# Performance work log

Measured on AMD Instinct MI355X. Metric: run time of the kernel, lower is better.

Reference implementation:

```python
import jax, jax.numpy as jnp
import numpy as np

T_SEG = 8      # n_segment
KSZ = 3        # LAM temporal kernel size
PAD = 1        # LAM temporal padding
BN_EPS = 1e-5


def setup_inputs() -> dict:
    key = jax.random.key(0)
    ks = jax.random.split(key, 12)
    n, t, c, h, w = 8, T_SEG, 256, 56, 56
    return {
        "x": jax.random.normal(ks[0], (n * t, c, h, w), jnp.float32),
        "net_w": jax.random.normal(ks[1], (c, c, 3, 3), jnp.float32) * 0.02,
        "net_b": jax.random.normal(ks[2], (c,), jnp.float32) * 0.02,
        "lam_w": jax.random.normal(ks[3], (c, c), jnp.float32) * 0.02,
        "lam_b": jax.random.normal(ks[4], (c,), jnp.float32) * 0.02,
        "mlp_w1": jax.random.normal(ks[5], (2 * t, t), jnp.float32) * 0.3,
        "bn_gamma": jax.random.uniform(ks[6], (2 * t,), jnp.float32, 0.5, 1.5),
        "bn_beta": jax.random.normal(ks[7], (2 * t,), jnp.float32) * 0.1,
        "bn_mean": jax.random.normal(ks[8], (2 * t,), jnp.float32) * 0.1,
        "bn_var": jax.random.uniform(ks[9], (2 * t,), jnp.float32, 0.5, 1.5),
        "mlp_w2": jax.random.normal(ks[10], (KSZ, 2 * t), jnp.float32) * 0.3,
        "me_w": jax.random.normal(ks[11], (3,), jnp.float32) * 0.3,
    }


def reference(x, net_w, net_b, lam_w, lam_b, mlp_w1, bn_gamma, bn_beta,
              bn_mean, bn_var, mlp_w2, me_w):
    t = T_SEG
    nt, c, h, w = x.shape
    n = nt // t

    # --- wrapped net: Conv2d 3x3, pad 1 ---
    out = jax.lax.conv_general_dilated(
        x, net_w, window_strides=(1, 1), padding="SAME",
        dimension_numbers=("NCHW", "OIHW", "NCHW"))
    out = out + net_b[None, :, None, None]

    # --- LAM ---
    new_x = out.reshape(n, t, c, h, w).transpose(0, 2, 1, 3, 4)  # (n,c,t,h,w)
    x_g = new_x.mean(axis=(2, 3, 4))                   # global pool -> (n,c)
    x_g = x_g @ lam_w.T + lam_b                        # Conv1d k=1 == matmul
    new_x = new_x + x_g[:, :, None, None, None]

    pooled = new_x.mean(axis=(3, 4)).reshape(n * c, t)  # per-(n,c) temporal sig
    hdn = pooled @ mlp_w1.T                              # (n*c, 2t), no bias
    hdn = (hdn - bn_mean) * (bn_gamma / jnp.sqrt(bn_var + BN_EPS)) + bn_beta
    hdn = jax.nn.relu(hdn)
    wgt = jax.nn.softmax(hdn @ mlp_w2.T, axis=-1).reshape(n, c, KSZ)

    # grouped conv2d (groups=n*c) == per-(n,c) depthwise temporal conv
    xpad = jnp.pad(new_x, ((0, 0), (0, 0), (PAD, PAD), (0, 0), (0, 0)))
    lam_out = sum(wgt[:, :, k, None, None, None] * xpad[:, :, k:k + t]
                  for k in range(KSZ))                  # (n,c,t,h,w)
    lam_out = lam_out.transpose(0, 2, 1, 3, 4).reshape(nt, c, h, w)

    # --- ME ---
    xv = lam_out.reshape(n, t, c, h, w)
    diff = xv[:, 1:] - xv[:, :-1]                       # frame differences
    diff = jnp.pad(diff, ((0, 0), (0, 1), (0, 0), (0, 0), (0, 0)))
    diff = diff.reshape(nt, c, h, w)
    y = diff.mean(axis=(2, 3))                          # (nt, c)
    ypad = jnp.pad(y, ((0, 0), (1, 1)))                 # conv1d over channel dim
    yc = sum(me_w[k] * ypad[:, k:k + c] for k in range(3))
    gate = jax.nn.sigmoid(yc)[:, :, None, None]

    return gate * lam_out
```

## Files before the change

kernel.cpp:

```cpp
#include <hip/hip_runtime.h>
#include <hip/hip_bf16.h>
#include <stdint.h>

#define AS1 __attribute__((address_space(1)))
#define AS3 __attribute__((address_space(3)))

typedef __attribute__((ext_vector_type(8))) short short8v;
typedef __attribute__((ext_vector_type(4))) float float4v;

#define NT 64
#define CCH 256
#define HH 56
#define WW 56
#define HWSZ 3136
#define HP 58
#define WP 58

#define OFF_XT   0ull
#define SZ_XT    110231552ull
#define OFF_WPK  (OFF_XT + SZ_XT)
#define SZ_WPK   1179648ull
#define OFF_CS   (OFF_WPK + SZ_WPK)
#define SZ_CS    65536ull
#define OFF_XG2  (OFF_CS + SZ_CS)
#define SZ_XG2   8192ull
#define OFF_WGT  (OFF_XG2 + SZ_XG2)
#define SZ_WGT   24576ull
#define OFF_M    (OFF_WGT + SZ_WGT)
#define SZ_M     65536ull
#define OFF_GATE (OFF_M + SZ_M)
#define SZ_GATE  65536ull

__device__ __forceinline__ unsigned short f2bf(float f) {
    unsigned int u = __float_as_uint(f);
    unsigned int r = (u + 0x7fffu + ((u >> 16) & 1u)) >> 16;
    return (unsigned short)r;
}

__device__ __forceinline__ void gload16(const unsigned short* g, unsigned short* l) {
    __builtin_amdgcn_global_load_lds((const AS1 void*)g, (AS3 void*)l, 16, 0, 0);
}

__global__ __launch_bounds__(256) void k0_transpose(const float* __restrict__ x,
                                                    unsigned short* __restrict__ xt) {
    int b = blockIdx.x;
    int cb = b & 3;
    int h  = (b >> 2) % 56;
    int nt = b / (4 * 56);
    int c0 = cb * 64;
    int tid = threadIdx.x;

    __shared__ float xs[64 * 57];

    const float* src = x + ((size_t)nt * CCH + c0) * HWSZ + h * WW;
    for (int li = tid; li < 896; li += 256) {
        int row = li / 14, f4 = li % 14;
        float4v v = *(const float4v*)(src + (size_t)row * HWSZ + f4 * 4);
        float* d = &xs[row * 57 + f4 * 4];
        d[0] = v.x; d[1] = v.y; d[2] = v.z; d[3] = v.w;
    }
    __syncthreads();

    unsigned short* dst = xt + (((size_t)nt * HP + (h + 1)) * WP) * CCH + c0;
    for (int job = tid; job < 464; job += 256) {
        int ww = job >> 3, cg = job & 7;
        short8v v;
        if (ww == 0 || ww == 57) {
            v = (short8v){0,0,0,0,0,0,0,0};
        } else {
            #pragma unroll
            for (int jj = 0; jj < 8; ++jj)
                v[jj] = (short)f2bf(xs[(cg * 8 + jj) * 57 + (ww - 1)]);
        }
        *(short8v*)(dst + ww * CCH + cg * 8) = v;
    }
    if (h == 0) {
        unsigned short* d0  = xt + ((size_t)nt * HP + 0)  * WP * CCH + c0;
        unsigned short* d57 = xt + ((size_t)nt * HP + 57) * WP * CCH + c0;
        short8v z = (short8v){0,0,0,0,0,0,0,0};
        for (int job = tid; job < 464; job += 256) {
            int ww = job >> 3, cg = job & 7;
            *(short8v*)(d0  + ww * CCH + cg * 8) = z;
            *(short8v*)(d57 + ww * CCH + cg * 8) = z;
        }
    }
}

__global__ __launch_bounds__(256) void kw_pack(const float* __restrict__ nw,
                                               unsigned short* __restrict__ wpk) {
    int idx = blockIdx.x * 256 + threadIdx.x;
    int rs = idx >> 16;
    int k  = (idx >> 8) & 255;
    int c  = idx & 255;
    wpk[idx] = f2bf(nw[(k * 256 + c) * 9 + rs]);
}


#define STGALL(bi_, tA_, tB_) do { \
    gload16(wpk + (tA_) + aoffg0, &lds[(bi_) * 8192 + ldsa0]); \
    gload16(wpk + (tA_) + aoffg1, &lds[(bi_) * 8192 + ldsa1]); \
    gload16(wpk + (tA_) + aoffg2, &lds[(bi_) * 8192 + ldsa2]); \
    gload16(wpk + (tA_) + aoffg3, &lds[(bi_) * 8192 + ldsa3]); \
    gload16(xt  + (tB_) + boffg0, &lds[24576 + (bi_) * 4096 + ldsb0]); \
    gload16(xt  + (tB_) + boffg1, &lds[24576 + (bi_) * 4096 + ldsb1]); \
} while (0)

#define LDAF(mi) (*(const short8v*)&lds[abase + (wm * 128 + (mi) * 16 + r16) * 32 + pA * 8])
#define LDBF(j)  (*(const short8v*)&lds[bbase + (wp * 64 + (j) * 16 + r16) * 32 + pA * 8])

#define BARSYNC do { \
    __builtin_amdgcn_s_barrier(); \
    __builtin_amdgcn_sched_barrier(0); \
} while (0)

__global__ __launch_bounds__(256, 2) void conv_mfma(const unsigned short* __restrict__ xt,
                                                    const unsigned short* __restrict__ wpk,
                                                    const float* __restrict__ net_b,
                                                    float* __restrict__ out,
                                                    float* __restrict__ chansum) {
    __shared__ unsigned short lds[36864];

    const int tid  = threadIdx.x;
    const int lane = tid & 63;
    const int wid  = tid >> 6;
    const int wm   = wid >> 1;
    const int wp   = wid & 1;
    const int r16  = lane & 15;
    const int hi   = lane >> 4;
    const int pA   = (hi + (r16 >> 1)) & 3;

    const int pblk = (blockIdx.x & 7) * 196 + (blockIdx.x >> 3);
    const int p0 = pblk * 128;

    int aoffg0, aoffg1, aoffg2, aoffg3;
    const int ldsa0 = tid * 8,        ldsa1 = (tid + 256) * 8;
    const int ldsa2 = (tid + 512) * 8, ldsa3 = (tid + 768) * 8;
    const int ldsb0 = tid * 8,        ldsb1 = (tid + 256) * 8;
    long boffg0, boffg1;
    {
        #pragma unroll
        for (int i = 0; i < 4; ++i) {
            int ch = tid + 256 * i;
            int r = ch >> 2;
            int cg = ((ch & 3) - (r >> 1)) & 3;
            int off = r * 256 + cg * 8;
            if (i == 0) aoffg0 = off; else if (i == 1) aoffg1 = off;
            else if (i == 2) aoffg2 = off; else aoffg3 = off;
        }
        #pragma unroll
        for (int i = 0; i < 2; ++i) {
            int ch = tid + 256 * i;
            int r = ch >> 2;
            int cg = ((ch & 3) - (r >> 1)) & 3;
            int p = p0 + r;
            int nt = p / HWSZ, hw = p - nt * HWSZ;
            int hh = hw / WW,  w  = hw - hh * WW;
            long off = ((long)(nt * HP + hh) * WP + w) * 256 + cg * 8;
            if (i == 0) boffg0 = off; else boffg1 = off;
        }
    }

    float4v acc[8][4];
    #pragma unroll
    for (int i = 0; i < 8; ++i)
        #pragma unroll
        for (int j = 0; j < 4; ++j) acc[i][j] = (float4v){0.f, 0.f, 0.f, 0.f};

    STGALL(0, 0, 0);
    STGALL(1, 32, 32);

    int cur = 0;
    for (int kt = 0; kt < 72; ++kt) {
        const int abase = cur * 8192;
        const int bbase = 24576 + cur * 4096;

        if (kt < 70) {
            const int ktn = kt + 2;
            int nb2 = cur + 2; if (nb2 >= 3) nb2 -= 3;
            const int rsn = ktn >> 3, con = (ktn & 7) * 32;
            const int tAn = rsn * 65536 + con;
            const int tBn = ((rsn / 3) * WP + (rsn - (rsn / 3) * 3)) * 256 + con;
            STGALL(nb2, tAn, tBn);
            asm volatile("s_waitcnt vmcnt(12)" ::: "memory");
        } else if (kt == 70) {
            asm volatile("s_waitcnt vmcnt(6)" ::: "memory");
        } else {
            asm volatile("s_waitcnt vmcnt(0)" ::: "memory");
        }
        BARSYNC;

        short8v afrag[8], bfrag[4];
        #pragma unroll
        for (int mi = 0; mi < 8; ++mi) afrag[mi] = LDAF(mi);
        #pragma unroll
        for (int j = 0; j < 4; ++j) bfrag[j] = LDBF(j);

        asm volatile("s_waitcnt lgkmcnt(0)" ::: "memory");
        __builtin_amdgcn_sched_barrier(0);
        __builtin_amdgcn_s_setprio(1);
        #pragma unroll
        for (int j = 0; j < 4; ++j)
            #pragma unroll
            for (int mi = 0; mi < 8; ++mi)
                acc[mi][j] = __builtin_amdgcn_mfma_f32_16x16x32_bf16(afrag[mi], bfrag[j], acc[mi][j], 0, 0, 0);
        __builtin_amdgcn_s_setprio(0);
        BARSYNC;

        ++cur; if (cur >= 3) cur = 0;
    }

    const int pw = p0 + wp * 64;
    const int ntw = pw / HWSZ;
    const int hwb = pw - ntw * HWSZ;
    #pragma unroll
    for (int mi = 0; mi < 8; ++mi) {
        #pragma unroll
        for (int r = 0; r < 4; ++r) {
            const int m = wm * 128 + mi * 16 + hi * 4 + r;
            const float bias = net_b[m];
            float csum = 0.f;
            float* orow = out + ((size_t)ntw * CCH + m) * HWSZ + hwb;
            #pragma unroll
            for (int j = 0; j < 4; ++j) {
                float v = acc[mi][j][r] + bias;
                orow[j * 16 + r16] = v;
                csum += v;
            }
            csum += __shfl_xor(csum, 1);
            csum += __shfl_xor(csum, 2);
            csum += __shfl_xor(csum, 4);
            csum += __shfl_xor(csum, 8);
            if (r16 == 0) atomicAdd(&chansum[ntw * CCH + m], csum);
        }
    }
}

__global__ __launch_bounds__(256) void k2_xg(const float* __restrict__ chansum,
                                             const float* __restrict__ lam_w,
                                             const float* __restrict__ lam_b,
                                             float* __restrict__ xg2) {
    int n = blockIdx.x, c = threadIdx.x;
    __shared__ float xs[256];
    float s = 0.f;
    #pragma unroll
    for (int t = 0; t < 8; ++t) s += chansum[(n * 8 + t) * CCH + c];
    xs[c] = s * (1.0f / (3136.f * 8.f));
    __syncthreads();
    float d = lam_b[c];
    const float* row = lam_w + c * 256;
    for (int cc = 0; cc < 256; ++cc) d += row[cc] * xs[cc];
    xg2[n * 256 + c] = d;
}

__global__ __launch_bounds__(256) void k3_wgt(const float* __restrict__ chansum,
                                              const float* __restrict__ xg2,
                                              const float* __restrict__ w1,
                                              const float* __restrict__ bg,
                                              const float* __restrict__ bb,
                                              const float* __restrict__ bm,
                                              const float* __restrict__ bv,
                                              const float* __restrict__ w2,
                                              float* __restrict__ wgt,
                                              float* __restrict__ mbuf) {
    int idx = blockIdx.x * 256 + threadIdx.x;
    int n = idx >> 8, c = idx & 255;
    float xg = xg2[idx];
    float p[8];
    #pragma unroll
    for (int t = 0; t < 8; ++t)
        p[t] = chansum[(n * 8 + t) * CCH + c] * (1.0f / 3136.f) + xg;
    float hd[16];
    #pragma unroll
    for (int j = 0; j < 16; ++j) {
        float s = 0.f;
        #pragma unroll
        for (int t = 0; t < 8; ++t) s += p[t] * w1[j * 8 + t];
        s = (s - bm[j]) * (bg[j] * rsqrtf(bv[j] + 1e-5f)) + bb[j];
        hd[j] = fmaxf(s, 0.f);
    }
    float lg[3];
    #pragma unroll
    for (int k = 0; k < 3; ++k) {
        float s = 0.f;
        #pragma unroll
        for (int j = 0; j < 16; ++j) s += hd[j] * w2[k * 16 + j];
        lg[k] = s;
    }
    float mx = fmaxf(fmaxf(lg[0], lg[1]), lg[2]);
    float e0 = expf(lg[0] - mx), e1 = expf(lg[1] - mx), e2 = expf(lg[2] - mx);
    float inv = 1.f / (e0 + e1 + e2);
    float wk[3] = {e0 * inv, e1 * inv, e2 * inv};
    #pragma unroll
    for (int k = 0; k < 3; ++k) wgt[idx * 3 + k] = wk[k];
    #pragma unroll
    for (int t = 0; t < 8; ++t) {
        float s = 0.f;
        #pragma unroll
        for (int k = 0; k < 3; ++k) {
            int tt = t + k - 1;
            if (tt >= 0 && tt < 8) s += wk[k] * p[tt];
        }
        mbuf[idx * 8 + t] = s;
    }
}

__global__ __launch_bounds__(256) void k4_gate(const float* __restrict__ mbuf,
                                               const float* __restrict__ me_w,
                                               float* __restrict__ gate) {
    int b = blockIdx.x;
    int n = b >> 3, t = b & 7;
    int c = threadIdx.x;
    __shared__ float y[256];
    float yv = 0.f;
    if (t < 7) yv = mbuf[(n * 256 + c) * 8 + t + 1] - mbuf[(n * 256 + c) * 8 + t];
    y[c] = yv;
    __syncthreads();
    float yc = me_w[1] * yv;
    if (c > 0)   yc += me_w[0] * y[c - 1];
    if (c < 255) yc += me_w[2] * y[c + 1];
    gate[b * 256 + c] = 1.f / (1.f + expf(-yc));
}

__global__ __launch_bounds__(256) void k5_final(float* __restrict__ out,
                                                const float* __restrict__ wgt,
                                                const float* __restrict__ xg2,
                                                const float* __restrict__ gate) {
    int tid = blockIdx.x * 256 + threadIdx.x;
    int hw4 = tid % 784;
    int nc = tid / 784;
    int n = nc >> 8, c = nc & 255;
    float w0 = wgt[nc * 3 + 0], w1 = wgt[nc * 3 + 1], w2 = wgt[nc * 3 + 2];
    float xg = xg2[nc];
    const size_t tstride = (size_t)CCH * HWSZ;
    size_t base = ((size_t)(n * 8) * CCH + c) * HWSZ + hw4 * 4;

    float4v o[8];
    #pragma unroll
    for (int t = 0; t < 8; ++t) o[t] = *(const float4v*)(out + base + t * tstride);

    #pragma unroll
    for (int t = 0; t < 8; ++t) {
        float g = gate[(n * 8 + t) * CCH + c];
        float4v lam;
        #pragma unroll
        for (int q = 0; q < 4; ++q) {
            float v = w1 * (o[t][q] + xg);
            if (t > 0) v += w0 * (o[t - 1][q] + xg);
            if (t < 7) v += w2 * (o[t + 1][q] + xg);
            lam[q] = g * v;
        }
        *(float4v*)(out + base + t * tstride) = lam;
    }
}

extern "C" void kernel_launch(void* const* d_in, const int* in_sizes, int n_in,
                              void* d_out, int out_size, void* d_ws, size_t ws_size,
                              hipStream_t stream) {
    const float* x      = (const float*)d_in[0];
    const float* net_w  = (const float*)d_in[1];
    const float* net_b  = (const float*)d_in[2];
    const float* lam_w  = (const float*)d_in[3];
    const float* lam_b  = (const float*)d_in[4];
    const float* mlp_w1 = (const float*)d_in[5];
    const float* bn_g   = (const float*)d_in[6];
    const float* bn_b   = (const float*)d_in[7];
    const float* bn_m   = (const float*)d_in[8];
    const float* bn_v   = (const float*)d_in[9];
    const float* mlp_w2 = (const float*)d_in[10];
    const float* me_w   = (const float*)d_in[11];
    float* out = (float*)d_out;

    char* ws = (char*)d_ws;
    unsigned short* xt  = (unsigned short*)(ws + OFF_XT);
    unsigned short* wpk = (unsigned short*)(ws + OFF_WPK);
    float* chansum = (float*)(ws + OFF_CS);
    float* xg2     = (float*)(ws + OFF_XG2);
    float* wgt     = (float*)(ws + OFF_WGT);
    float* mbuf    = (float*)(ws + OFF_M);
    float* gate    = (float*)(ws + OFF_GATE);

    hipMemsetAsync(chansum, 0, SZ_CS, stream);
    kw_pack<<<2304, 256, 0, stream>>>(net_w, wpk);
    k0_transpose<<<64 * 56 * 4, 256, 0, stream>>>(x, xt);
    conv_mfma<<<1568, 256, 0, stream>>>(xt, wpk, net_b, out, chansum);
    k2_xg<<<8, 256, 0, stream>>>(chansum, lam_w, lam_b, xg2);
    k3_wgt<<<8, 256, 0, stream>>>(chansum, xg2, mlp_w1, bn_g, bn_b, bn_m, bn_v, mlp_w2, wgt, mbuf);
    k4_gate<<<64, 256, 0, stream>>>(mbuf, me_w, gate);
    k5_final<<<6272, 256, 0, stream>>>(out, wgt, xg2, gate);
}
```

Baseline: 443.0 us.

## Load conv B operand directly to registers and double-buffer A fragments

The implicit-GEMM conv main loop no longer stages the activation (B) tile through LDS. Each lane loads its B fragments straight from global memory into registers one tile ahead. A fragments are also read from LDS one tile ahead into ping-pong register sets, so LDS reads overlap the MFMAs. This cuts LDS usage and LDS traffic, but raises register pressure and makes B loads uncoalesced per-lane 16-byte gathers with no LDS reuse across waves.

```diff
diff --git a/kernel.cpp b/kernel.cpp
--- a/kernel.cpp
+++ b/kernel.cpp
@@ -96,19 +96,48 @@
 }
 
 
-#define STGALL(bi_, tA_, tB_) do { \
-    gload16(wpk + (tA_) + aoffg0, &lds[(bi_) * 8192 + ldsa0]); \
-    gload16(wpk + (tA_) + aoffg1, &lds[(bi_) * 8192 + ldsa1]); \
-    gload16(wpk + (tA_) + aoffg2, &lds[(bi_) * 8192 + ldsa2]); \
-    gload16(wpk + (tA_) + aoffg3, &lds[(bi_) * 8192 + ldsa3]); \
-    gload16(xt  + (tB_) + boffg0, &lds[24576 + (bi_) * 4096 + ldsb0]); \
-    gload16(xt  + (tB_) + boffg1, &lds[24576 + (bi_) * 4096 + ldsb1]); \
+#define STGA(sl_, tA_) do { \
+    gload16(wpk + (tA_) + aoffg0, &lds[(sl_) * 8192 + ldsa0]); \
+    gload16(wpk + (tA_) + aoffg1, &lds[(sl_) * 8192 + ldsa1]); \
+    gload16(wpk + (tA_) + aoffg2, &lds[(sl_) * 8192 + ldsa2]); \
+    gload16(wpk + (tA_) + aoffg3, &lds[(sl_) * 8192 + ldsa3]); \
 } while (0)
 
-#define LDAF(mi) (*(const short8v*)&lds[abase + (wm * 128 + (mi) * 16 + r16) * 32 + pA * 8])
-#define LDBF(j)  (*(const short8v*)&lds[bbase + (wp * 64 + (j) * 16 + r16) * 32 + pA * 8])
-
-#define BARSYNC do { \
+#define LDAF(sl_, mi) (*(const short8v*)&lds[(sl_) * 8192 + (wm * 128 + (mi) * 16 + r16) * 32 + pA * 8])
+
+#define VMWAIT_(n) asm volatile("s_waitcnt vmcnt(" #n ")" ::: "memory")
+#define VMWAIT(n) VMWAIT_(n)
+
+#define TILE(ACUR, ANXT, BCUR, BNXT, kt_, sl_, HAS2, HAS1, VMC) do { \
+    if (HAS2) { \
+        int sl2 = (sl_) + 2; if (sl2 >= 3) sl2 -= 3; \
+        const int ktn2 = (kt_) + 2; \
+        STGA(sl2, (ktn2 >> 3) * 65536 + (ktn2 & 7) * 32); \
+    } \
+    if (HAS1) { \
+        const int ktn1 = (kt_) + 1; \
+        const int rsn = ktn1 >> 3, con = (ktn1 & 7) * 32; \
+        const int tBn = ((rsn / 3) * WP + (rsn - (rsn / 3) * 3)) * 256 + con; \
+        BNXT[0] = *(const short8v*)(xt + bAddr0 + tBn); \
+        BNXT[1] = *(const short8v*)(xt + bAddr1 + tBn); \
+        BNXT[2] = *(const short8v*)(xt + bAddr2 + tBn); \
+        BNXT[3] = *(const short8v*)(xt + bAddr3 + tBn); \
+    } \
+    VMWAIT(VMC); \
+    __builtin_amdgcn_s_barrier(); \
+    __builtin_amdgcn_sched_barrier(0); \
+    if (HAS1) { \
+        int sl1 = (sl_) + 1; if (sl1 >= 3) sl1 -= 3; \
+        _Pragma("unroll") \
+        for (int mi = 0; mi < 8; ++mi) ANXT[mi] = LDAF(sl1, mi); \
+    } \
+    __builtin_amdgcn_s_setprio(1); \
+    _Pragma("unroll") \
+    for (int j = 0; j < 4; ++j) \
+        _Pragma("unroll") \
+        for (int mi = 0; mi < 8; ++mi) \
+            acc[mi][j] = __builtin_amdgcn_mfma_f32_16x16x32_bf16(ACUR[mi], BCUR[j], acc[mi][j], 0, 0, 0); \
+    __builtin_amdgcn_s_setprio(0); \
     __builtin_amdgcn_s_barrier(); \
     __builtin_amdgcn_sched_barrier(0); \
 } while (0)
@@ -118,7 +147,7 @@
                                                     const float* __restrict__ net_b,
                                                     float* __restrict__ out,
                                                     float* __restrict__ chansum) {
-    __shared__ unsigned short lds[36864];
+    __shared__ unsigned short lds[24576];
 
     const int tid  = threadIdx.x;
     const int lane = tid & 63;
@@ -133,10 +162,8 @@
     const int p0 = pblk * 128;
 
     int aoffg0, aoffg1, aoffg2, aoffg3;
-    const int ldsa0 = tid * 8,        ldsa1 = (tid + 256) * 8;
+    const int ldsa0 = tid * 8,         ldsa1 = (tid + 256) * 8;
     const int ldsa2 = (tid + 512) * 8, ldsa3 = (tid + 768) * 8;
-    const int ldsb0 = tid * 8,        ldsb1 = (tid + 256) * 8;
-    long boffg0, boffg1;
     {
         #pragma unroll
         for (int i = 0; i < 4; ++i) {
@@ -147,16 +174,18 @@
             if (i == 0) aoffg0 = off; else if (i == 1) aoffg1 = off;
             else if (i == 2) aoffg2 = off; else aoffg3 = off;
         }
-        #pragma unroll
-        for (int i = 0; i < 2; ++i) {
-            int ch = tid + 256 * i;
-            int r = ch >> 2;
-            int cg = ((ch & 3) - (r >> 1)) & 3;
-            int p = p0 + r;
+    }
+
+    int bAddr0, bAddr1, bAddr2, bAddr3;
+    {
+        #pragma unroll
+        for (int j = 0; j < 4; ++j) {
+            int p = p0 + wp * 64 + j * 16 + r16;
             int nt = p / HWSZ, hw = p - nt * HWSZ;
             int hh = hw / WW,  w  = hw - hh * WW;
-            long off = ((long)(nt * HP + hh) * WP + w) * 256 + cg * 8;
-            if (i == 0) boffg0 = off; else boffg1 = off;
+            int off = ((nt * HP + hh) * WP + w) * 256 + hi * 8;
+            if (j == 0) bAddr0 = off; else if (j == 1) bAddr1 = off;
+            else if (j == 2) bAddr2 = off; else bAddr3 = off;
         }
     }
 
@@ -166,48 +195,30 @@
         #pragma unroll
         for (int j = 0; j < 4; ++j) acc[i][j] = (float4v){0.f, 0.f, 0.f, 0.f};
 
-    STGALL(0, 0, 0);
-    STGALL(1, 32, 32);
-
-    int cur = 0;
-    for (int kt = 0; kt < 72; ++kt) {
-        const int abase = cur * 8192;
-        const int bbase = 24576 + cur * 4096;
-
-        if (kt < 70) {
-            const int ktn = kt + 2;
-            int nb2 = cur + 2; if (nb2 >= 3) nb2 -= 3;
-            const int rsn = ktn >> 3, con = (ktn & 7) * 32;
-            const int tAn = rsn * 65536 + con;
-            const int tBn = ((rsn / 3) * WP + (rsn - (rsn / 3) * 3)) * 256 + con;
-            STGALL(nb2, tAn, tBn);
-            asm volatile("s_waitcnt vmcnt(12)" ::: "memory");
-        } else if (kt == 70) {
-            asm volatile("s_waitcnt vmcnt(6)" ::: "memory");
-        } else {
-            asm volatile("s_waitcnt vmcnt(0)" ::: "memory");
-        }
-        BARSYNC;
-
-        short8v afrag[8], bfrag[4];
-        #pragma unroll
-        for (int mi = 0; mi < 8; ++mi) afrag[mi] = LDAF(mi);
-        #pragma unroll
-        for (int j = 0; j < 4; ++j) bfrag[j] = LDBF(j);
-
-        asm volatile("s_waitcnt lgkmcnt(0)" ::: "memory");
-        __builtin_amdgcn_sched_barrier(0);
-        __builtin_amdgcn_s_setprio(1);
-        #pragma unroll
-        for (int j = 0; j < 4; ++j)
-            #pragma unroll
-            for (int mi = 0; mi < 8; ++mi)
-                acc[mi][j] = __builtin_amdgcn_mfma_f32_16x16x32_bf16(afrag[mi], bfrag[j], acc[mi][j], 0, 0, 0);
-        __builtin_amdgcn_s_setprio(0);
-        BARSYNC;
-
-        ++cur; if (cur >= 3) cur = 0;
-    }
+    short8v AX[8], AY[8], BX[4], BY[4];
+
+    STGA(0, 0);
+    STGA(1, 32);
+    BX[0] = *(const short8v*)(xt + bAddr0);
+    BX[1] = *(const short8v*)(xt + bAddr1);
+    BX[2] = *(const short8v*)(xt + bAddr2);
+    BX[3] = *(const short8v*)(xt + bAddr3);
+    VMWAIT(8);
+    __builtin_amdgcn_s_barrier();
+    __builtin_amdgcn_sched_barrier(0);
+    #pragma unroll
+    for (int mi = 0; mi < 8; ++mi) AX[mi] = LDAF(0, mi);
+
+    int sl = 0;
+    for (int t2 = 0; t2 < 70; t2 += 2) {
+        TILE(AX, AY, BX, BY, t2, sl, true, true, 12);
+        sl = (sl == 2) ? 0 : sl + 1;
+        TILE(AY, AX, BY, BX, t2 + 1, sl, true, true, 12);
+        sl = (sl == 2) ? 0 : sl + 1;
+    }
+    TILE(AX, AY, BX, BY, 70, sl, false, true, 8);
+    sl = (sl == 2) ? 0 : sl + 1;
+    TILE(AY, AX, BY, BX, 71, sl, false, false, 0);
 
     const int pw = p0 + wp * 64;
     const int ntw = pw / HWSZ;
```

Result: slower. 565.4 us (+27.6%).
